# Kernel tuning notes

Hardware: AMD Instinct MI355X
Metric: run time of the kernel (lower is better)

The kernel has to match this reference:

```python
import jax, jax.numpy as jnp
from jax import lax
import numpy as np

B = 512          # batch
M = 2000         # num_memories
CC = 16          # conv_channel_size
F = CC * 4 * 6 * 6  # 2304 feature size
BN_EPS = 1e-5
COS_EPS = 1e-8
SHRINK_EPS = 0.01


def conv(x, w, b, stride, pad):
    y = lax.conv_general_dilated(x, w, (stride, stride), [(pad, pad), (pad, pad)],
                                 dimension_numbers=('NCHW', 'OIHW', 'NCHW'))
    return y + b[None, :, None, None]


def deconv(x, w, b, stride, pad, out_pad):
    # w is torch ConvTranspose2d layout: (in, out, kh, kw)
    k = w.shape[2]
    w2 = jnp.flip(w, (2, 3)).transpose(1, 0, 2, 3)  # (out, in, kh, kw)
    p = [(k - 1 - pad, k - 1 - pad + out_pad)] * 2
    y = lax.conv_general_dilated(x, w2, (1, 1), p, lhs_dilation=(stride, stride),
                                 dimension_numbers=('NCHW', 'OIHW', 'NCHW'))
    return y + b[None, :, None, None]


def bn(x, g, b):
    # BatchNorm2d in training mode: per-channel batch statistics (biased var)
    m = x.mean((0, 2, 3), keepdims=True)
    v = x.var((0, 2, 3), keepdims=True)
    return g[None, :, None, None] * (x - m) * lax.rsqrt(v + BN_EPS) + b[None, :, None, None]


def setup_inputs() -> dict:
    key = jax.random.key(0)
    ks = jax.random.split(key, 16)
    rn = lambda k, s, sc=0.05: jax.random.normal(k, s, jnp.float32) * sc
    return {
        'x': jax.random.uniform(ks[0], (B, 1, 96, 96), jnp.float32),
        'c1_w': rn(ks[1], (16, 1, 1, 1), 0.3), 'c1_b': jnp.zeros(16),
        'bn1_g': jnp.ones(16), 'bn1_b': jnp.zeros(16),
        'c2_w': rn(ks[2], (32, 16, 3, 3)), 'c2_b': jnp.zeros(32),
        'bn2_g': jnp.ones(32), 'bn2_b': jnp.zeros(32),
        'c3_w': rn(ks[3], (64, 32, 3, 3)), 'c3_b': jnp.zeros(64),
        'bn3_g': jnp.ones(64), 'bn3_b': jnp.zeros(64),
        'c4_w': rn(ks[4], (64, 64, 3, 3)), 'c4_b': jnp.zeros(64),
        'bn4_g': jnp.ones(64), 'bn4_b': jnp.zeros(64),
        'memory': rn(ks[5], (M, F), 0.03),
        'd0_w': rn(ks[6], (64, 64, 3, 3)), 'd0_b': jnp.zeros(64),
        'dbn0_g': jnp.ones(64), 'dbn0_b': jnp.zeros(64),
        'd1_w': rn(ks[7], (64, 32, 3, 3)), 'd1_b': jnp.zeros(32),
        'dbn1_g': jnp.ones(32), 'dbn1_b': jnp.zeros(32),
        'd2_w': rn(ks[8], (32, 16, 2, 2)), 'd2_b': jnp.zeros(16),
        'dbn2_g': jnp.ones(16), 'dbn2_b': jnp.zeros(16),
        'd3_w': rn(ks[9], (16, 1, 2, 2)), 'd3_b': jnp.zeros(1),
    }


def reference(x, c1_w, c1_b, bn1_g, bn1_b, c2_w, c2_b, bn2_g, bn2_b,
              c3_w, c3_b, bn3_g, bn3_b, c4_w, c4_b, bn4_g, bn4_b, memory,
              d0_w, d0_b, dbn0_g, dbn0_b, d1_w, d1_b, dbn1_g, dbn1_b,
              d2_w, d2_b, dbn2_g, dbn2_b, d3_w, d3_b):
    relu = jax.nn.relu
    # Encoder: 96 -> 49 -> 25 -> 13 -> 6
    h = relu(bn(conv(x, c1_w, c1_b, 2, 1), bn1_g, bn1_b))
    h = relu(bn(conv(h, c2_w, c2_b, 2, 1), bn2_g, bn2_b))
    h = relu(bn(conv(h, c3_w, c3_b, 2, 1), bn3_g, bn3_b))
    h = relu(bn(conv(h, c4_w, c4_b, 2, 0), bn4_g, bn4_b))
    z = h.reshape(h.shape[0], -1)  # (B, 2304)

    # Memory addressing: cosine similarity without materializing (B, M, F)
    zn = jnp.linalg.norm(z, axis=1)          # (B,)
    mn = jnp.linalg.norm(memory, axis=1)     # (M,)
    sim = (z @ memory.T) / jnp.maximum(zn[:, None] * mn[None, :], COS_EPS)
    w = jax.nn.softmax(sim, axis=1)
    # Sparse hard-shrink addressing + L1 renorm
    t = 1.0 / memory.shape[0]
    w = relu(w - t) * w / (jnp.abs(w - t) + SHRINK_EPS)
    w = w / jnp.sum(jnp.abs(w), axis=1, keepdims=True)
    z_hat = w @ memory  # (B, F)

    # Decoder: 6 -> 13 -> 25 -> 49 -> 98
    g = z_hat.reshape(-1, 64, 6, 6)
    g = relu(bn(deconv(g, d0_w, d0_b, 2, 0, 0), dbn0_g, dbn0_b))
    g = relu(bn(deconv(g, d1_w, d1_b, 2, 1, 0), dbn1_g, dbn1_b))
    g = relu(bn(deconv(g, d2_w, d2_b, 2, 1, 1), dbn2_g, dbn2_b))
    g = jax.nn.sigmoid(deconv(g, d3_w, d3_b, 2, 0, 0))
    return g
```

## Files before the change

kernel.cpp:

```cpp
#include <hip/hip_runtime.h>
#include <stdint.h>


typedef unsigned short ushort_t;
typedef __bf16 bf16x8 __attribute__((ext_vector_type(8)));
typedef float f32x4 __attribute__((ext_vector_type(4)));

#define DEV static __device__ __forceinline__

DEV ushort_t f2bf(float f){
  union { float f; uint32_t u; } v; v.f = f;
  return (ushort_t)((v.u + 0x7FFFu + ((v.u >> 16) & 1u)) >> 16);
}
DEV float bf2f(ushort_t u){
  union { uint32_t u; float f; } v; v.u = ((uint32_t)u) << 16;
  return v.f;
}

DEV uint32_t affine2(uint32_t rw, const float* ac, int ci, int nch){
  float lo = bf2f((ushort_t)(rw & 0xffffu));
  float hi = bf2f((ushort_t)(rw >> 16));
  lo = fmaxf(fmaf(ac[ci],   lo, ac[nch+ci]),   0.f);
  hi = fmaxf(fmaf(ac[ci+1], hi, ac[nch+ci+1]), 0.f);
  return (uint32_t)f2bf(lo) | ((uint32_t)f2bf(hi) << 16);
}
DEV uint4 stage_chunk(uint4 raw, const float* ac, int ci0, int nch){
  uint4 o;
  o.x = affine2(raw.x, ac, ci0+0, nch);
  o.y = affine2(raw.y, ac, ci0+2, nch);
  o.z = affine2(raw.z, ac, ci0+4, nch);
  o.w = affine2(raw.w, ac, ci0+6, nch);
  return o;
}

#define H_XS   0
#define H_S2   64
#define H_Q2   96
#define H_S3   192
#define H_Q3   256
#define H_S4   448
#define H_Q4   512
#define H_DS0  704
#define H_DQ0  768
#define H_DS1  960
#define H_DQ1  992
#define H_DS2  1088
#define H_DQ2  1104
#define H_ZN   1152
#define H_MN   1664
#define H_BUK  4096
#define NBUK   16
#define BSTRIDE 1280
#define HDR_FLOATS (H_BUK + NBUK*BSTRIDE)

#define OW2 0
#define OW3 5120
#define OW4 23552
#define OD0 60416
#define OD1 97280
#define OD2 115712
#define NWPK 117760

#define SIMSTRIDE 1024000
#define ZHSTRIDE  1179648
#define NSPL 4

#define PREP_XS 256
#define PREP_W2 (PREP_XS + 460)
#define PREP_TOT (PREP_W2 + 4536)

DEV float* bkt(float* hdr, int blk){ return hdr + H_BUK + (size_t)(blk & (NBUK-1))*BSTRIDE; }

DEV void coef_lds(const float* __restrict__ hdr, int offS, int offQ,
                  const float* __restrict__ g, const float* __restrict__ be,
                  float* ac, int nch, float invN, int tid){
  if (tid < nch){
    float s = 0.f, q = 0.f;
    #pragma unroll
    for (int k=0;k<NBUK;k++){
      s += hdr[H_BUK + k*BSTRIDE + offS + tid];
      q += hdr[H_BUK + k*BSTRIDE + offQ + tid];
    }
    float m = s*invN;
    float v = q*invN - m*m;
    float a = g[tid]*rsqrtf(v + 1e-5f);
    ac[tid] = a;
    ac[nch+tid] = be[tid] - m*a;
  }
}

__global__ __launch_bounds__(256) void k_prep(
    const float* __restrict__ mem, ushort_t* __restrict__ mbf, ushort_t* __restrict__ mt,
    float* __restrict__ hdr,
    const float* __restrict__ c2w, const float* __restrict__ c3w, const float* __restrict__ c4w,
    const float* __restrict__ d0w, const float* __restrict__ d1w, const float* __restrict__ d2w,
    ushort_t* __restrict__ WPK, const float* __restrict__ x){
  __shared__ float sm[32*33];
  const int blk = blockIdx.x, tid = threadIdx.x;
  if (blk < PREP_XS){
    float s = 0.f, q = 0.f;
    const int total = 512*49*49;
    for (int idx = blk*256 + tid; idx < total; idx += 256*256){
      int b = idx / 2401;
      int r = idx - b*2401;
      int i = r / 49, j = r - i*49;
      float v = 0.f;
      if (i > 0 && j > 0) v = x[(size_t)b*9216 + (2*i-1)*96 + (2*j-1)];
      s += v; q += v*v;
    }
    for (int o=32;o;o>>=1){ s += __shfl_down(s,o,64); q += __shfl_down(q,o,64); }
    int w = tid>>6;
    if ((tid&63)==0){ sm[w*2]=s; sm[w*2+1]=q; }
    __syncthreads();
    if (tid==0){
      float* bk = bkt(hdr, blk);
      atomicAdd(&bk[H_XS+0], sm[0]+sm[2]+sm[4]+sm[6]);
      atomicAdd(&bk[H_XS+1], sm[1]+sm[3]+sm[5]+sm[7]);
    }
  } else if (blk < PREP_W2){
    int i = (blk - PREP_XS)*256 + tid;
    if (i >= NWPK) return;
    float val = 0.f;
    if (i < OW3){
      int co = i/160, k = i - co*160, tap = k>>4, ci = k&15;
      if (tap < 9) val = c2w[(co*16+ci)*9+tap];
    } else if (i < OW4){
      int r = i - OW3; int co = r/288, k = r - co*288, tap = k>>5, ci = k&31;
      val = c3w[(co*32+ci)*9+tap];
    } else if (i < OD0){
      int r = i - OW4; int co = r/576, k = r - co*576, tap = k>>6, ci = k&63;
      val = c4w[(co*64+ci)*9+tap];
    } else if (i < OD1){
      int r = i - OD0;
      const int base[4]={0,16384,24576,32768}, K[4]={256,128,128,64};
      const int T0[4][4] = {{0,2,6,8},{1,7,0,0},{3,5,0,0},{4,0,0,0}};
      int cl = (r<16384)?0:(r<24576)?1:(r<32768)?2:3;
      int rr = r - base[cl]; int co = rr/K[cl], k = rr - co*K[cl], t = k>>6, ci = k&63;
      val = d0w[(ci*64+co)*9 + T0[cl][t]];
    } else if (i < OD2){
      int r = i - OD1;
      const int base[4]={0,2048,6144,10240}, K[4]={64,128,128,256};
      const int T1[4][4] = {{4,0,0,0},{3,5,0,0},{1,7,0,0},{0,2,6,8}};
      int cl = (r<2048)?0:(r<6144)?1:(r<10240)?2:3;
      int rr = r - base[cl]; int co = rr/K[cl], k = rr - co*K[cl], t = k>>6, ci = k&63;
      val = d1w[(ci*32+co)*9 + T1[cl][t]];
    } else {
      int r = i - OD2;
      int cl = r>>9, s = r&511, co = s>>5, ci = s&31;
      const int pis[4]={0,0,1,1}, pjs[4]={0,1,0,1};
      val = d2w[((ci*16+co)*2 + (1-pis[cl]))*2 + (1-pjs[cl])];
    }
    WPK[i] = f2bf(val);
  } else {
    const int mb = blk - PREP_W2;
    const int ft = mb % 72, mtile = mb / 72;
    const int tx = tid & 31, ty = tid >> 5;
    #pragma unroll
    for (int r0=0;r0<4;r0++){
      int m = mtile*32 + r0*8 + ty;
      int f = ft*32 + tx;
      float v = (m < 2000) ? mem[(size_t)m*2304 + f] : 0.f;
      sm[(r0*8+ty)*33 + tx] = v;
      if (m < 2000) mbf[(size_t)m*2304 + f] = f2bf(v);
      float p = v*v;
      for (int o=16;o;o>>=1) p += __shfl_down(p, o, 32);
      if (tx==0 && m<2000) atomicAdd(&hdr[H_MN+m], p);
    }
    __syncthreads();
    #pragma unroll
    for (int r0=0;r0<4;r0++){
      int f = ft*32 + r0*8 + ty;
      mt[(size_t)f*2016 + mtile*32 + tx] = f2bf(sm[tx*33 + r0*8+ty]);
    }
  }
}

__global__ __launch_bounds__(256) void k_conv2m(
    const float* __restrict__ x, const ushort_t* __restrict__ WPK, const float* __restrict__ b2g,
    const float* __restrict__ c1w, const float* __restrict__ c1b,
    const float* __restrict__ bn1g, const float* __restrict__ bn1b,
    float* __restrict__ hdr, ushort_t* __restrict__ out){
  __shared__ ushort_t inp[27*51*16];
  __shared__ float ac[32];
  const int blk = blockIdx.x, b = blk>>1, h = blk&1, tid = threadIdx.x;
  const int ro = h*13, nr = h?12:13, npos = nr*25, ntiles = (npos+15)>>4;
  if (tid < 16){
    float sx=0.f, qx=0.f;
    #pragma unroll
    for (int k=0;k<NBUK;k++){ sx += hdr[H_BUK+k*BSTRIDE+H_XS]; qx += hdr[H_BUK+k*BSTRIDE+H_XS+1]; }
    const float N = 512.f*49.f*49.f;
    float mx = sx/N, vx = qx/N - mx*mx;
    float mean = c1w[tid]*mx + c1b[tid];
    float a = bn1g[tid]*rsqrtf(c1w[tid]*c1w[tid]*vx + 1e-5f);
    ac[tid] = a*c1w[tid];
    ac[16+tid] = a*(c1b[tid]-mean) + bn1b[tid];
  }
  __syncthreads();
  for (int e = tid; e < 27*51; e += 256){
    int lr = e/51, gc = e - lr*51;
    int grg = 2*ro + lr;
    bool inside = (grg>=1 && grg<=49 && gc>=1 && gc<=49);
    float v = 0.f;
    if (grg>=2 && grg<=49 && gc>=2 && gc<=49) v = x[(size_t)b*9216 + (2*grg-3)*96 + (2*gc-3)];
    ushort_t hv[16];
    if (inside){
      #pragma unroll
      for (int c=0;c<16;c++) hv[c] = f2bf(fmaxf(fmaf(ac[c], v, ac[16+c]), 0.f));
    } else {
      #pragma unroll
      for (int c=0;c<16;c++) hv[c] = 0;
    }
    uint32_t w0[8];
    #pragma unroll
    for (int c=0;c<8;c++) w0[c] = (uint32_t)hv[2*c] | ((uint32_t)hv[2*c+1]<<16);
    uint4* dst = (uint4*)&inp[e*16];
    dst[0] = make_uint4(w0[0],w0[1],w0[2],w0[3]);
    dst[1] = make_uint4(w0[4],w0[5],w0[6],w0[7]);
  }
  __syncthreads();
  const int wv = tid>>6, lane = tid&63, r = lane&15, q = lane>>4;
  const int cotile = wv&1;
  bf16x8 af[5];
  #pragma unroll
  for (int c=0;c<5;c++) af[c] = *(const bf16x8*)(WPK + OW2 + (cotile*16+r)*160 + c*32 + q*8);
  float biasr[4];
  #pragma unroll
  for (int v=0;v<4;v++) biasr[v] = b2g[cotile*16 + q*4 + v];
  const int TOFF[10] = {0,1,2,51,52,53,102,103,104,0};
  const int qhi = q>>1, ci0 = (q&1)*8;
  float sacc[4]={0,0,0,0}, qacc[4]={0,0,0,0};
  for (int t = wv>>1; t < ntiles; t += 2){
    int p = t*16 + r;
    bool ok = p < npos;
    int pc = ok ? p : 0;
    int a_ = pc/25, c_ = pc - a_*25;
    int pb = (2*a_)*51 + 2*c_;
    f32x4 acc = {0.f,0.f,0.f,0.f};
    #pragma unroll
    for (int c=0;c<5;c++){
      int toff = qhi ? TOFF[2*c+1] : TOFF[2*c];
      bf16x8 bv = *(const bf16x8*)&inp[(pb + toff)*16 + ci0];
      acc = __builtin_amdgcn_mfma_f32_16x16x32_bf16(af[c], bv, acc, 0, 0, 0);
    }
    if (ok){
      int pg = (ro + a_)*25 + c_;
      ushort_t pk[4];
      #pragma unroll
      for (int reg=0;reg<4;reg++){
        float y = acc[reg] + biasr[reg];
        pk[reg] = f2bf(y);
        sacc[reg] += y; qacc[reg] += y*y;
      }
      *(uint2*)&out[((size_t)b*625 + pg)*32 + cotile*16 + q*4] =
        make_uint2((uint32_t)pk[0] | ((uint32_t)pk[1]<<16), (uint32_t)pk[2] | ((uint32_t)pk[3]<<16));
    }
  }
  float* bk = bkt(hdr, blk);
  #pragma unroll
  for (int reg=0;reg<4;reg++){
    float s = sacc[reg], qq = qacc[reg];
    for (int o=8;o;o>>=1){ s += __shfl_down(s,o,16); qq += __shfl_down(qq,o,16); }
    if (r==0){ atomicAdd(&bk[H_S2+cotile*16+q*4+reg], s); atomicAdd(&bk[H_Q2+cotile*16+q*4+reg], qq); }
  }
}

__global__ __launch_bounds__(256) void k_conv3m(
    const ushort_t* __restrict__ h2, const ushort_t* __restrict__ WPK, const float* __restrict__ b3g,
    const float* __restrict__ g, const float* __restrict__ be,
    float* __restrict__ hdr, ushort_t* __restrict__ out){
  __shared__ ushort_t inp[15*27*32];
  __shared__ float ac[64];
  const int blk = blockIdx.x, b = blk>>1, h = blk&1, tid = threadIdx.x;
  const int a0 = h*7, na = h?6:7, npos = na*13, ntiles = (npos+15)>>4, nrows = 2*na+1;
  coef_lds(hdr, H_S2, H_Q2, g, be, ac, 32, 1.f/(512.f*625.f), tid);
  __syncthreads();
  for (int e = tid; e < nrows*27*4; e += 256){
    int cell = e>>2, ch = e&3;
    int lr = cell/27, lc = cell - lr*27;
    int ii = 2*a0 - 1 + lr, j = lc - 1;
    uint4 val = make_uint4(0,0,0,0);
    if ((unsigned)ii < 25u && (unsigned)j < 25u){
      uint4 raw = *(const uint4*)&h2[((size_t)b*625 + ii*25 + j)*32 + ch*8];
      val = stage_chunk(raw, ac, ch*8, 32);
    }
    int slot = ch ^ ((cell>>1)&3);
    *(uint4*)&inp[cell*32 + slot*8] = val;
  }
  __syncthreads();
  const int wv = tid>>6, lane = tid&63, r = lane&15, q = lane>>4;
  bf16x8 af[9];
  #pragma unroll
  for (int c=0;c<9;c++) af[c] = *(const bf16x8*)(WPK + OW3 + (wv*16+r)*288 + c*32 + q*8);
  float biasr[4];
  #pragma unroll
  for (int v=0;v<4;v++) biasr[v] = b3g[wv*16 + q*4 + v];
  const int TOFF[9] = {0,1,2,27,28,29,54,55,56};
  float sacc[4]={0,0,0,0}, qacc[4]={0,0,0,0};
  for (int t = 0; t < ntiles; t++){
    int p = t*16 + r;
    bool ok = p < npos;
    int pc = ok ? p : 0;
    int a_ = pc/13, c_ = pc - a_*13;
    int pb = (2*a_)*27 + 2*c_;
    f32x4 acc = {0.f,0.f,0.f,0.f};
    #pragma unroll
    for (int c=0;c<9;c++){
      int cell = pb + TOFF[c];
      int slot = q ^ ((cell>>1)&3);
      bf16x8 bv = *(const bf16x8*)&inp[cell*32 + slot*8];
      acc = __builtin_amdgcn_mfma_f32_16x16x32_bf16(af[c], bv, acc, 0, 0, 0);
    }
    if (ok){
      int pos = (a0 + a_)*13 + c_;
      ushort_t pk[4];
      #pragma unroll
      for (int reg=0;reg<4;reg++){
        float y = acc[reg] + biasr[reg];
        pk[reg] = f2bf(y);
        sacc[reg] += y; qacc[reg] += y*y;
      }
      *(uint2*)&out[((size_t)b*169 + pos)*64 + wv*16 + q*4] =
        make_uint2((uint32_t)pk[0] | ((uint32_t)pk[1]<<16), (uint32_t)pk[2] | ((uint32_t)pk[3]<<16));
    }
  }
  float* bk = bkt(hdr, blk);
  #pragma unroll
  for (int reg=0;reg<4;reg++){
    float s = sacc[reg], qq = qacc[reg];
    for (int o=8;o;o>>=1){ s += __shfl_down(s,o,16); qq += __shfl_down(qq,o,16); }
    if (r==0){ atomicAdd(&bk[H_S3+wv*16+q*4+reg], s); atomicAdd(&bk[H_Q3+wv*16+q*4+reg], qq); }
  }
}

__global__ __launch_bounds__(256) void k_conv4m(
    const ushort_t* __restrict__ h3, const ushort_t* __restrict__ WPK, const float* __restrict__ b4g,
    const float* __restrict__ g, const float* __restrict__ be,
    float* __restrict__ hdr, float* __restrict__ out){
  __shared__ ushort_t inp[169*64];
  __shared__ float ac[128];
  const int b = blockIdx.x, tid = threadIdx.x;
  coef_lds(hdr, H_S3, H_Q3, g, be, ac, 64, 1.f/(512.f*169.f), tid);
  __syncthreads();
  for (int e = tid; e < 169*8; e += 256){
    int cell = e>>3, ch = e&7;
    uint4 raw = *(const uint4*)&h3[((size_t)b*169 + cell)*64 + ch*8];
    uint4 val = stage_chunk(raw, ac, ch*8, 64);
    int slot = ch ^ ((cell>>1)&7);
    *(uint4*)&inp[cell*64 + slot*8] = val;
  }
  __syncthreads();
  const int wv = tid>>6, lane = tid&63, r = lane&15, q = lane>>4;
  bf16x8 af[18];
  #pragma unroll
  for (int c=0;c<18;c++) af[c] = *(const bf16x8*)(WPK + OW4 + (wv*16+r)*576 + c*32 + q*8);
  float biasr[4];
  #pragma unroll
  for (int v=0;v<4;v++) biasr[v] = b4g[wv*16 + q*4 + v];
  const int TOFF[9] = {0,1,2,13,14,15,26,27,28};
  float sacc[4]={0,0,0,0}, qacc[4]={0,0,0,0};
  for (int t = 0; t < 3; t++){
    int p = t*16 + r;
    bool ok = p < 36;
    int pc = ok ? p : 0;
    int a_ = pc/6, c_ = pc - a_*6;
    int pb = (2*a_)*13 + 2*c_;
    f32x4 acc = {0.f,0.f,0.f,0.f};
    #pragma unroll
    for (int c=0;c<18;c++){
      int cell = pb + TOFF[c>>1];
      int chunk = (c&1)*4 + q;
      int slot = chunk ^ ((cell>>1)&7);
      bf16x8 bv = *(const bf16x8*)&inp[cell*64 + slot*8];
      acc = __builtin_amdgcn_mfma_f32_16x16x32_bf16(af[c], bv, acc, 0, 0, 0);
    }
    if (ok){
      #pragma unroll
      for (int reg=0;reg<4;reg++){
        float y = acc[reg] + biasr[reg];
        out[((size_t)b*64 + wv*16 + q*4 + reg)*36 + p] = y;
        sacc[reg] += y; qacc[reg] += y*y;
      }
    }
  }
  float* bk = bkt(hdr, b);
  #pragma unroll
  for (int reg=0;reg<4;reg++){
    float s = sacc[reg], qq = qacc[reg];
    for (int o=8;o;o>>=1){ s += __shfl_down(s,o,16); qq += __shfl_down(qq,o,16); }
    if (r==0){ atomicAdd(&bk[H_S4+wv*16+q*4+reg], s); atomicAdd(&bk[H_Q4+wv*16+q*4+reg], qq); }
  }
}

__global__ __launch_bounds__(256) void k_gemmA(
    const float* __restrict__ ZR, const ushort_t* __restrict__ Bm, float* __restrict__ D,
    const float* __restrict__ g, const float* __restrict__ be, float* __restrict__ hdr){
  __shared__ __align__(16) ushort_t lB[128*40];
  __shared__ __align__(16) ushort_t lA[128*40];
  __shared__ float ac[128];
  const int blk = blockIdx.x;
  const int s = blk >> 6, t = blk & 63;
  const int bi = t >> 4, bj = t & 15;
  const int m0 = bi*128, n0 = bj*128;
  const int k0 = s*18, k1 = k0 + 18;
  const int tid = threadIdx.x;
  coef_lds(hdr, H_S4, H_Q4, g, be, ac, 64, 1.f/(512.f*36.f), tid);
  const int lane = tid & 63, wv = tid >> 6;
  const int r = lane & 15, q = lane >> 4;
  const int wr = wv >> 1, wc = wv & 1;
  const bool bj0 = (bj == 0);
  float* Ds = D + (size_t)s*SIMSTRIDE;
  const int srow = tid >> 1, skq = (tid & 1) * 16;
  const bool bok = (n0 + srow) < 2000;
  const ushort_t* pb = Bm + (size_t)(n0 + srow)*2304 + skq;
  const float*    pa = ZR + (size_t)(m0 + srow)*2304 + skq;
  uint4* wB = (uint4*)&lB[srow*40 + skq];
  uint4* wA = (uint4*)&lA[srow*40 + skq];
  const uint4 zz = make_uint4(0,0,0,0);
  uint4 rb0 = bok ? *(const uint4*)(pb + (size_t)k0*32)     : zz;
  uint4 rb1 = bok ? *(const uint4*)(pb + (size_t)k0*32 + 8) : zz;
  f32x4 raA[4];
  #pragma unroll
  for (int i=0;i<4;i++) raA[i] = *(const f32x4*)(pa + (size_t)k0*32 + i*4);
  f32x4 acc[4][4];
  #pragma unroll
  for (int i=0;i<4;i++)
    #pragma unroll
    for (int j=0;j<4;j++) acc[i][j] = (f32x4){0.f,0.f,0.f,0.f};
  float zsq = 0.f;
  __syncthreads();
  for (int k=k0; k<k1; k++){
    if (k > k0) __syncthreads();
    wB[0] = rb0; wB[1] = rb1;
    {
      const int kb = k*32 + skq;
      uint32_t pw[8];
      #pragma unroll
      for (int jj=0;jj<8;jj++){
        float v0 = raA[jj>>1][(jj&1)*2+0];
        float v1 = raA[jj>>1][(jj&1)*2+1];
        int c0 = (kb + 2*jj) / 36;
        int c1 = (kb + 2*jj + 1) / 36;
        float h0 = fmaxf(fmaf(ac[c0], v0, ac[64+c0]), 0.f);
        float h1 = fmaxf(fmaf(ac[c1], v1, ac[64+c1]), 0.f);
        if (bj0) zsq += h0*h0 + h1*h1;
        pw[jj] = (uint32_t)f2bf(h0) | ((uint32_t)f2bf(h1) << 16);
      }
      wA[0] = make_uint4(pw[0],pw[1],pw[2],pw[3]);
      wA[1] = make_uint4(pw[4],pw[5],pw[6],pw[7]);
    }
    if (k+1 < k1){
      const ushort_t* nb = pb + (size_t)(k+1)*32;
      rb0 = bok ? *(const uint4*)(nb)     : zz;
      rb1 = bok ? *(const uint4*)(nb + 8) : zz;
      const float* na = pa + (size_t)(k+1)*32;
      #pragma unroll
      for (int i=0;i<4;i++) raA[i] = *(const f32x4*)(na + i*4);
    }
    __syncthreads();
    bf16x8 aF[4], bF[4];
    #pragma unroll
    for (int mt=0;mt<4;mt++) aF[mt] = *(const bf16x8*)&lA[(wr*64+mt*16+r)*40 + q*8];
    #pragma unroll
    for (int nt=0;nt<4;nt++) bF[nt] = *(const bf16x8*)&lB[(wc*64+nt*16+r)*40 + q*8];
    #pragma unroll
    for (int mt=0;mt<4;mt++)
      #pragma unroll
      for (int nt=0;nt<4;nt++)
        acc[mt][nt] = __builtin_amdgcn_mfma_f32_16x16x32_bf16(aF[mt], bF[nt], acc[mt][nt], 0, 0, 0);
  }
  if (bj0){
    zsq += __shfl_down(zsq, 1, 64);
    if ((tid & 1) == 0) atomicAdd(&hdr[H_ZN + m0 + srow], zsq);
  }
  #pragma unroll
  for (int mt=0;mt<4;mt++){
    int row = m0 + wr*64 + mt*16 + q*4;
    #pragma unroll
    for (int nt=0;nt<4;nt++){
      int col = n0 + wc*64 + nt*16 + r;
      if (col < 2000){
        #pragma unroll
        for (int reg=0;reg<4;reg++)
          Ds[(size_t)(row+reg)*2000 + col] = acc[mt][nt][reg];
      }
    }
  }
}

__global__ __launch_bounds__(256) void k_gemmB(const ushort_t* __restrict__ A, const ushort_t* __restrict__ Bm,
                                               float* __restrict__ D, int Nb, int N, int Kp, int kch,
                                               int tiles, int ksp, size_t dstride){
  __shared__ __align__(16) ushort_t lB[128*40];
  const int blk = blockIdx.x;
  const int s = blk / tiles, t = blk - s*tiles;
  const int bi = t / Nb, bj = t - bi*Nb;
  const int m0 = bi*128, n0 = bj*128;
  const int k0 = s*ksp, k1 = min(kch, k0 + ksp);
  const int tid = threadIdx.x;
  const int lane = tid & 63, wv = tid >> 6;
  const int r = lane & 15, q = lane >> 4;
  const int wr = wv >> 1, wc = wv & 1;
  float* Ds = D + (size_t)s*dstride;
  const int srow = tid >> 1, skq = (tid & 1) * 16;
  const bool bok = (n0 + srow) < N;
  const ushort_t* pb = Bm + (size_t)(n0 + srow)*Kp + skq;
  uint4* wB = (uint4*)&lB[srow*40 + skq];
  const uint4 zz = make_uint4(0,0,0,0);
  uint4 rb0 = bok ? *(const uint4*)(pb + k0*32)     : zz;
  uint4 rb1 = bok ? *(const uint4*)(pb + k0*32 + 8) : zz;
  const ushort_t* pa = A + (size_t)(m0 + wr*64 + r)*Kp + q*8;
  bf16x8 aN[4];
  #pragma unroll
  for (int mt=0;mt<4;mt++) aN[mt] = *(const bf16x8*)(pa + k0*32 + (size_t)(mt*16)*Kp);
  f32x4 acc[4][4];
  #pragma unroll
  for (int i=0;i<4;i++)
    #pragma unroll
    for (int j=0;j<4;j++) acc[i][j] = (f32x4){0.f,0.f,0.f,0.f};
  for (int k=k0; k<k1; k++){
    if (k > k0) __syncthreads();
    wB[0] = rb0; wB[1] = rb1;
    bf16x8 aF[4];
    #pragma unroll
    for (int mt=0;mt<4;mt++) aF[mt] = aN[mt];
    if (k+1 < k1){
      const ushort_t* nb = pb + (k+1)*32;
      rb0 = bok ? *(const uint4*)(nb)     : zz;
      rb1 = bok ? *(const uint4*)(nb + 8) : zz;
      const ushort_t* na = pa + (k+1)*32;
      #pragma unroll
      for (int mt=0;mt<4;mt++) aN[mt] = *(const bf16x8*)(na + (size_t)(mt*16)*Kp);
    }
    __syncthreads();
    bf16x8 bF[4];
    #pragma unroll
    for (int nt=0;nt<4;nt++) bF[nt] = *(const bf16x8*)&lB[(wc*64+nt*16+r)*40 + q*8];
    #pragma unroll
    for (int mt=0;mt<4;mt++)
      #pragma unroll
      for (int nt=0;nt<4;nt++)
        acc[mt][nt] = __builtin_amdgcn_mfma_f32_16x16x32_bf16(aF[mt], bF[nt], acc[mt][nt], 0, 0, 0);
  }
  #pragma unroll
  for (int mt=0;mt<4;mt++){
    int row = m0 + wr*64 + mt*16 + q*4;
    #pragma unroll
    for (int nt=0;nt<4;nt++){
      int col = n0 + wc*64 + nt*16 + r;
      if (col < N){
        #pragma unroll
        for (int reg=0;reg<4;reg++)
          Ds[(size_t)(row+reg)*N + col] = acc[mt][nt][reg];
      }
    }
  }
}

__global__ __launch_bounds__(256) void k_softmax(const float* __restrict__ sim, float* __restrict__ hdr,
                                                 ushort_t* __restrict__ wbf){
  __shared__ float e[2000];
  __shared__ float red[8];
  const int b = blockIdx.x, tid = threadIdx.x;
  const float znb = sqrtf(hdr[H_ZN+b]);
  float part = 0.f;
  for (int m=tid;m<2000;m+=256){
    size_t ix = (size_t)b*2000+m;
    float sv = 0.f;
    #pragma unroll
    for (int j=0;j<NSPL;j++) sv += sim[ix + (size_t)j*SIMSTRIDE];
    float mnb = sqrtf(hdr[H_MN+m]);
    float s = sv / fmaxf(znb * mnb, 1e-8f);
    float ev = __expf(s);
    e[m] = ev; part += ev;
  }
  for (int o=32;o;o>>=1) part += __shfl_down(part,o,64);
  if ((tid&63)==0) red[tid>>6] = part;
  __syncthreads();
  const float denom = red[0]+red[1]+red[2]+red[3];
  const float t = 1.0f/2000.0f;
  float part2 = 0.f;
  for (int m=tid;m<2000;m+=256){
    float w = e[m]/denom;
    float d = w - t;
    float sh = fmaxf(d,0.f)*w/(fabsf(d)+0.01f);
    e[m] = sh; part2 += sh;
  }
  for (int o=32;o;o>>=1) part2 += __shfl_down(part2,o,64);
  if ((tid&63)==0) red[4+(tid>>6)] = part2;
  __syncthreads();
  const float inv = 1.0f/(red[4]+red[5]+red[6]+red[7]);
  for (int m=tid;m<2016;m+=256){
    ushort_t o = 0;
    if (m < 2000) o = f2bf(e[m]*inv);
    wbf[(size_t)b*2016+m] = o;
  }
}

__global__ __launch_bounds__(256) void k_deconv0m(
    const float* __restrict__ zh, const ushort_t* __restrict__ WPK, const float* __restrict__ b0g,
    float* __restrict__ hdr, ushort_t* __restrict__ out){
  __shared__ ushort_t inp[64*64];
  const int b = blockIdx.x, tid = threadIdx.x;
  for (int i = tid; i < 512; i += 256) ((uint4*)inp)[i] = make_uint4(0,0,0,0);
  __syncthreads();
  for (int i = tid; i < 576; i += 256){
    int idx = i*4;
    f32x4 v = *(const f32x4*)&zh[(size_t)b*2304 + idx];
    #pragma unroll
    for (int j=1;j<NSPL;j++)
      v += *(const f32x4*)&zh[(size_t)b*2304 + idx + (size_t)j*ZHSTRIDE];
    int ci = idx/36;
    int p  = idx - ci*36;
    int chunk = ci >> 3, cil = ci & 7;
    #pragma unroll
    for (int e2=0;e2<4;e2++){
      int pp = p + e2;
      int r6 = pp/6, c6 = pp - r6*6;
      int cell = (r6+1)*8 + (c6+1);
      int slot = chunk ^ ((cell>>1)&7);
      inp[cell*64 + slot*8 + cil] = f2bf(v[e2]);
    }
  }
  __syncthreads();
  const int wv = tid>>6, lane = tid&63, r = lane&15, q = lane>>4;
  float biasr[4];
  #pragma unroll
  for (int v=0;v<4;v++) biasr[v] = b0g[wv*16 + q*4 + v];
  const int NCOL[4]={7,6,7,6}, NPOS[4]={49,42,42,36}, NT[4]={4,3,3,3},
            NCH[4]={8,4,4,2}, KB[4]={0,16384,24576,32768}, KK[4]={256,128,128,64},
            PI[4]={0,0,1,1}, PJ[4]={0,1,0,1};
  const int TOFF[4][4] = {{9,8,1,0},{9,1,0,0},{9,8,0,0},{9,0,0,0}};
  float sacc[4]={0,0,0,0}, qacc[4]={0,0,0,0};
  #pragma unroll
  for (int cl=0; cl<4; cl++){
    bf16x8 af[8];
    #pragma unroll
    for (int m=0;m<NCH[cl];m++)
      af[m] = *(const bf16x8*)(WPK + OD0 + KB[cl] + (wv*16+r)*KK[cl] + m*32 + q*8);
    for (int t = 0; t < NT[cl]; t++){
      int p = t*16 + r;
      bool ok = p < NPOS[cl];
      int pc = ok ? p : 0;
      int a_ = pc/NCOL[cl], c_ = pc - a_*NCOL[cl];
      int pb = a_*8 + c_;
      f32x4 acc = {0.f,0.f,0.f,0.f};
      #pragma unroll
      for (int m=0;m<NCH[cl];m++){
        int cell = pb + TOFF[cl][m>>1];
        int chunk = (m&1)*4 + q;
        int slot = chunk ^ ((cell>>1)&7);
        bf16x8 bv = *(const bf16x8*)&inp[cell*64 + slot*8];
        acc = __builtin_amdgcn_mfma_f32_16x16x32_bf16(af[m], bv, acc, 0, 0, 0);
      }
      if (ok){
        int pos = (2*a_+PI[cl])*13 + (2*c_+PJ[cl]);
        ushort_t pk[4];
        #pragma unroll
        for (int reg=0;reg<4;reg++){
          float y = acc[reg] + biasr[reg];
          pk[reg] = f2bf(y);
          sacc[reg] += y; qacc[reg] += y*y;
        }
        *(uint2*)&out[((size_t)b*169 + pos)*64 + wv*16 + q*4] =
          make_uint2((uint32_t)pk[0] | ((uint32_t)pk[1]<<16), (uint32_t)pk[2] | ((uint32_t)pk[3]<<16));
      }
    }
  }
  float* bk = bkt(hdr, b);
  #pragma unroll
  for (int reg=0;reg<4;reg++){
    float s = sacc[reg], qq = qacc[reg];
    for (int o=8;o;o>>=1){ s += __shfl_down(s,o,16); qq += __shfl_down(qq,o,16); }
    if (r==0){ atomicAdd(&bk[H_DS0+wv*16+q*4+reg], s); atomicAdd(&bk[H_DQ0+wv*16+q*4+reg], qq); }
  }
}

__global__ __launch_bounds__(256) void k_deconv1m(
    const ushort_t* __restrict__ g0, const ushort_t* __restrict__ WPK, const float* __restrict__ b1g,
    const float* __restrict__ g, const float* __restrict__ be,
    float* __restrict__ hdr, ushort_t* __restrict__ out){
  __shared__ ushort_t inp[169*64];
  __shared__ float ac[128];
  const int b = blockIdx.x, tid = threadIdx.x;
  coef_lds(hdr, H_DS0, H_DQ0, g, be, ac, 64, 1.f/(512.f*169.f), tid);
  __syncthreads();
  for (int e = tid; e < 169*8; e += 256){
    int cell = e>>3, ch = e&7;
    uint4 raw = *(const uint4*)&g0[((size_t)b*169 + cell)*64 + ch*8];
    uint4 val = stage_chunk(raw, ac, ch*8, 64);
    int slot = ch ^ ((cell>>1)&7);
    *(uint4*)&inp[cell*64 + slot*8] = val;
  }
  __syncthreads();
  const int wv = tid>>6, lane = tid&63, r = lane&15, q = lane>>4;
  const int cotile = wv&1, ph = wv>>1;
  float biasr[4];
  #pragma unroll
  for (int v=0;v<4;v++) biasr[v] = b1g[cotile*16 + q*4 + v];
  const int NCOL[4]={13,12,13,12}, NPOS[4]={169,156,156,144}, NT[4]={11,10,10,9},
            NCH[4]={2,4,4,8}, KB[4]={0,2048,6144,10240}, KK[4]={64,128,128,256},
            PI[4]={0,0,1,1}, PJ[4]={0,1,0,1};
  const int TOFF[4][4] = {{0,0,0,0},{1,0,0,0},{13,0,0,0},{14,13,1,0}};
  float sacc[4]={0,0,0,0}, qacc[4]={0,0,0,0};
  #pragma unroll
  for (int cl=0; cl<4; cl++){
    bf16x8 af[8];
    #pragma unroll
    for (int m=0;m<NCH[cl];m++)
      af[m] = *(const bf16x8*)(WPK + OD1 + KB[cl] + (cotile*16+r)*KK[cl] + m*32 + q*8);
    for (int t = ph; t < NT[cl]; t += 2){
      int p = t*16 + r;
      bool ok = p < NPOS[cl];
      int pc = ok ? p : 0;
      int a_ = pc/NCOL[cl], c_ = pc - a_*NCOL[cl];
      int pb = a_*13 + c_;
      f32x4 acc = {0.f,0.f,0.f,0.f};
      #pragma unroll
      for (int m=0;m<NCH[cl];m++){
        int cell = pb + TOFF[cl][m>>1];
        int chunk = (m&1)*4 + q;
        int slot = chunk ^ ((cell>>1)&7);
        bf16x8 bv = *(const bf16x8*)&inp[cell*64 + slot*8];
        acc = __builtin_amdgcn_mfma_f32_16x16x32_bf16(af[m], bv, acc, 0, 0, 0);
      }
      if (ok){
        int pos = (2*a_+PI[cl])*25 + (2*c_+PJ[cl]);
        ushort_t pk[4];
        #pragma unroll
        for (int reg=0;reg<4;reg++){
          float y = acc[reg] + biasr[reg];
          pk[reg] = f2bf(y);
          sacc[reg] += y; qacc[reg] += y*y;
        }
        *(uint2*)&out[((size_t)b*625 + pos)*32 + cotile*16 + q*4] =
          make_uint2((uint32_t)pk[0] | ((uint32_t)pk[1]<<16), (uint32_t)pk[2] | ((uint32_t)pk[3]<<16));
      }
    }
  }
  float* bk = bkt(hdr, b);
  #pragma unroll
  for (int reg=0;reg<4;reg++){
    float s = sacc[reg], qq = qacc[reg];
    for (int o=8;o;o>>=1){ s += __shfl_down(s,o,16); qq += __shfl_down(qq,o,16); }
    if (r==0){ atomicAdd(&bk[H_DS1+cotile*16+q*4+reg], s); atomicAdd(&bk[H_DQ1+cotile*16+q*4+reg], qq); }
  }
}

__global__ __launch_bounds__(256) void k_deconv2m(
    const ushort_t* __restrict__ g1, const ushort_t* __restrict__ WPK, const float* __restrict__ bg,
    const float* __restrict__ g, const float* __restrict__ be,
    float* __restrict__ hdr, ushort_t* __restrict__ out){
  __shared__ ushort_t inp[625*32];
  __shared__ float ac[64];
  const int b = blockIdx.x, tid = threadIdx.x;
  coef_lds(hdr, H_DS1, H_DQ1, g, be, ac, 32, 1.f/(512.f*625.f), tid);
  __syncthreads();
  for (int e = tid; e < 625*4; e += 256){
    int cell = e>>2, ch = e&3;
    uint4 raw = *(const uint4*)&g1[((size_t)b*625 + cell)*32 + ch*8];
    uint4 val = stage_chunk(raw, ac, ch*8, 32);
    int slot = ch ^ ((cell>>1)&3);
    *(uint4*)&inp[cell*32 + slot*8] = val;
  }
  __syncthreads();
  const int wv = tid>>6, lane = tid&63, r = lane&15, q = lane>>4;
  const int cl = wv;
  float biasr[4];
  #pragma unroll
  for (int v=0;v<4;v++) biasr[v] = bg[q*4 + v];
  const int NCOL[4]={25,24,25,24}, NPOS[4]={625,600,600,576}, NT[4]={40,38,38,36},
            TOFF[4]={0,1,25,26};
  const int nc = NCOL[cl], npos = NPOS[cl], nt = NT[cl], toff = TOFF[cl];
  bf16x8 af = *(const bf16x8*)(WPK + OD2 + cl*512 + r*32 + q*8);
  float sacc[4]={0,0,0,0}, qacc[4]={0,0,0,0};
  for (int t = 0; t < nt; t++){
    int p = t*16 + r;
    bool ok = p < npos;
    int pc = ok ? p : 0;
    int a_ = pc/nc, c_ = pc - a_*nc;
    int cell = a_*25 + c_ + toff;
    int slot = q ^ ((cell>>1)&3);
    f32x4 acc = {0.f,0.f,0.f,0.f};
    bf16x8 bv = *(const bf16x8*)&inp[cell*32 + slot*8];
    acc = __builtin_amdgcn_mfma_f32_16x16x32_bf16(af, bv, acc, 0, 0, 0);
    if (ok){
      #pragma unroll
      for (int reg=0;reg<4;reg++){
        float y = acc[reg] + biasr[reg];
        out[((size_t)(b*16 + q*4 + reg)*4 + cl)*625 + p] = f2bf(y);
        sacc[reg] += y; qacc[reg] += y*y;
      }
    }
  }
  float* bk = bkt(hdr, b);
  #pragma unroll
  for (int reg=0;reg<4;reg++){
    float s = sacc[reg], qq = qacc[reg];
    for (int o=8;o;o>>=1){ s += __shfl_down(s,o,16); qq += __shfl_down(qq,o,16); }
    if (r==0){ atomicAdd(&bk[H_DS2+q*4+reg], s); atomicAdd(&bk[H_DQ2+q*4+reg], qq); }
  }
}

__global__ __launch_bounds__(256) void k_deconv3(const ushort_t* __restrict__ g2, const float* __restrict__ w,
                                                 const float* __restrict__ bias,
                                                 const float* __restrict__ g, const float* __restrict__ be,
                                                 float* __restrict__ hdr, float* __restrict__ out){
  __shared__ float ac[32];
  __shared__ float wl[64];
  const int tid = threadIdx.x;
  coef_lds(hdr, H_DS2, H_DQ2, g, be, ac, 16, 1.f/(512.f*2401.f), tid);
  if (tid >= 64 && tid < 128) wl[tid-64] = w[tid-64];
  __syncthreads();
  int idx = blockIdx.x*256 + tid;
  if (idx >= 512*2401) return;
  int b = idx / 2401; int loc = idx - b*2401;
  int ii = loc / 49, jj = loc - ii*49;
  int pi = ii & 1, pj = jj & 1, cl = pi*2 + pj;
  int a = ii >> 1, c = jj >> 1;
  int nc = pj ? 24 : 25;
  const float b0 = bias[0];
  float acc00 = b0, acc01 = b0, acc10 = b0, acc11 = b0;
  const ushort_t* gp = g2 + ((size_t)(b*16)*4 + cl)*625 + a*nc + c;
  #pragma unroll
  for (int ci=0; ci<16; ci++){
    float raw = bf2f(gp[(size_t)ci*4*625]);
    float h = fmaxf(fmaf(ac[ci], raw, ac[16+ci]), 0.f);
    acc00 = fmaf(h, wl[ci*4+0], acc00);
    acc01 = fmaf(h, wl[ci*4+1], acc01);
    acc10 = fmaf(h, wl[ci*4+2], acc10);
    acc11 = fmaf(h, wl[ci*4+3], acc11);
  }
  float* op = out + (size_t)b*9604 + (2*ii)*98 + 2*jj;
  op[0]   = 1.f/(1.f + __expf(-acc00));
  op[1]   = 1.f/(1.f + __expf(-acc01));
  op[98]  = 1.f/(1.f + __expf(-acc10));
  op[99]  = 1.f/(1.f + __expf(-acc11));
}

extern "C" void kernel_launch(void* const* d_in, const int* in_sizes, int n_in,
                              void* d_out, int out_size, void* d_ws, size_t ws_size,
                              hipStream_t stream){
  (void)in_sizes; (void)n_in; (void)out_size; (void)ws_size;
  const float* x     = (const float*)d_in[0];
  const float* c1w   = (const float*)d_in[1];
  const float* c1b   = (const float*)d_in[2];
  const float* bn1g  = (const float*)d_in[3];
  const float* bn1b  = (const float*)d_in[4];
  const float* c2w   = (const float*)d_in[5];
  const float* c2b   = (const float*)d_in[6];
  const float* bn2g  = (const float*)d_in[7];
  const float* bn2b  = (const float*)d_in[8];
  const float* c3w   = (const float*)d_in[9];
  const float* c3b   = (const float*)d_in[10];
  const float* bn3g  = (const float*)d_in[11];
  const float* bn3b  = (const float*)d_in[12];
  const float* c4w   = (const float*)d_in[13];
  const float* c4b   = (const float*)d_in[14];
  const float* bn4g  = (const float*)d_in[15];
  const float* bn4b  = (const float*)d_in[16];
  const float* mem   = (const float*)d_in[17];
  const float* d0w   = (const float*)d_in[18];
  const float* d0b   = (const float*)d_in[19];
  const float* dbn0g = (const float*)d_in[20];
  const float* dbn0b = (const float*)d_in[21];
  const float* d1w   = (const float*)d_in[22];
  const float* d1b   = (const float*)d_in[23];
  const float* dbn1g = (const float*)d_in[24];
  const float* dbn1b = (const float*)d_in[25];
  const float* d2w   = (const float*)d_in[26];
  const float* d2b   = (const float*)d_in[27];
  const float* dbn2g = (const float*)d_in[28];
  const float* dbn2b = (const float*)d_in[29];
  const float* d3w   = (const float*)d_in[30];
  const float* d3b   = (const float*)d_in[31];

  float* hdr  = (float*)d_ws;
  float* H2f  = hdr + HDR_FLOATS;
  float* H3f  = H2f + 10240000;
  float* ZRAW = H3f + 5537792;
  float* WSLOT= ZRAW + 1179648;
  float* G2   = WSLOT + 73728;
  ushort_t* MEMBF = (ushort_t*)(G2 + 19668992);
  ushort_t* MEMT  = MEMBF + 4608000;
  ushort_t* ZBF   = MEMT + 4644864;
  ushort_t* WBF   = ZBF + 1179648;
  ushort_t* WPK   = (ushort_t*)WSLOT;
  float* SIMP = G2;
  float* ZHP  = G2 + NSPL*SIMSTRIDE;
  ushort_t* G2BF = (ushort_t*)G2;
  ushort_t* H2CL = (ushort_t*)H2f;
  ushort_t* H3CL = (ushort_t*)H3f;
  ushort_t* G0CL = (ushort_t*)H3f;
  ushort_t* G1CL = (ushort_t*)H2f;
  float* OUT = (float*)d_out;

  hipMemsetAsync(hdr, 0, HDR_FLOATS*sizeof(float), stream);
  k_prep     <<<PREP_TOT, 256, 0, stream>>>(mem, MEMBF, MEMT, hdr,
                                            c2w, c3w, c4w, d0w, d1w, d2w, WPK, x);
  k_conv2m   <<<1024, 256, 0, stream>>>(x, WPK, c2b, c1w, c1b, bn1g, bn1b, hdr, H2CL);
  k_conv3m   <<<1024, 256, 0, stream>>>(H2CL, WPK, c3b, bn2g, bn2b, hdr, H3CL);
  k_conv4m   <<<512, 256, 0, stream>>>(H3CL, WPK, c4b, bn3g, bn3b, hdr, ZRAW);
  k_gemmA    <<<256, 256, 0, stream>>>(ZRAW, MEMBF, SIMP, bn4g, bn4b, hdr);
  k_softmax  <<<512, 256, 0, stream>>>(SIMP, hdr, WBF);
  k_gemmB    <<<288, 256, 0, stream>>>(WBF, MEMT, ZHP, 18, 2304, 2016, 63, 72, 16, ZHSTRIDE);
  k_deconv0m <<<512, 256, 0, stream>>>(ZHP, WPK, d0b, hdr, G0CL);
  k_deconv1m <<<512, 256, 0, stream>>>(G0CL, WPK, d1b, dbn0g, dbn0b, hdr, G1CL);
  k_deconv2m <<<512, 256, 0, stream>>>(G1CL, WPK, d2b, dbn1g, dbn1b, hdr, G2BF);
  k_deconv3  <<<4802, 256, 0, stream>>>(G2BF, d3w, d3b, dbn2g, dbn2b, hdr, OUT);
}
```

Measured before the change: 346.2 us.

## Vectorize memory prep transpose and switch deconv2 output to channel-last layout

The memory prep kernel now reads four floats per thread, packs them to bf16 before staging in shared memory, and handles 128-feature tiles per block, so fewer blocks are launched and global accesses are wider. The deconv2 output is changed from channel-planar to position-major with 16 channels contiguous. This lets deconv2 write 8-byte packed stores and lets the final deconv read all 16 channels with two 16-byte loads instead of 16 strided scalar loads. The transpose step still does 2-byte scalar global stores, and the shared-memory reads in that loop may hit bank conflicts.

```diff
diff --git a/kernel.cpp b/kernel.cpp
--- a/kernel.cpp
+++ b/kernel.cpp
@@ -67,7 +67,7 @@
 
 #define PREP_XS 256
 #define PREP_W2 (PREP_XS + 460)
-#define PREP_TOT (PREP_W2 + 4536)
+#define PREP_TOT (PREP_W2 + 63*18)
 
 DEV float* bkt(float* hdr, int blk){ return hdr + H_BUK + (size_t)(blk & (NBUK-1))*BSTRIDE; }
 
@@ -95,9 +95,10 @@
     const float* __restrict__ c2w, const float* __restrict__ c3w, const float* __restrict__ c4w,
     const float* __restrict__ d0w, const float* __restrict__ d1w, const float* __restrict__ d2w,
     ushort_t* __restrict__ WPK, const float* __restrict__ x){
-  __shared__ float sm[32*33];
+  __shared__ ushort_t smu[32*132];
   const int blk = blockIdx.x, tid = threadIdx.x;
   if (blk < PREP_XS){
+    float* sm = (float*)smu;
     float s = 0.f, q = 0.f;
     const int total = 512*49*49;
     for (int idx = blk*256 + tid; idx < total; idx += 256*256){
@@ -153,24 +154,27 @@
     WPK[i] = f2bf(val);
   } else {
     const int mb = blk - PREP_W2;
-    const int ft = mb % 72, mtile = mb / 72;
+    const int ft = mb % 18, mtile = mb / 18;
     const int tx = tid & 31, ty = tid >> 5;
     #pragma unroll
     for (int r0=0;r0<4;r0++){
       int m = mtile*32 + r0*8 + ty;
-      int f = ft*32 + tx;
-      float v = (m < 2000) ? mem[(size_t)m*2304 + f] : 0.f;
-      sm[(r0*8+ty)*33 + tx] = v;
-      if (m < 2000) mbf[(size_t)m*2304 + f] = f2bf(v);
-      float p = v*v;
+      int f = ft*128 + tx*4;
+      f32x4 v = {0.f,0.f,0.f,0.f};
+      if (m < 2000) v = *(const f32x4*)&mem[(size_t)m*2304 + f];
+      ushort_t h0=f2bf(v[0]), h1=f2bf(v[1]), h2=f2bf(v[2]), h3=f2bf(v[3]);
+      uint2 pk = make_uint2((uint32_t)h0 | ((uint32_t)h1<<16), (uint32_t)h2 | ((uint32_t)h3<<16));
+      *(uint2*)&smu[(r0*8+ty)*132 + tx*4] = pk;
+      if (m < 2000) *(uint2*)&mbf[(size_t)m*2304 + f] = pk;
+      float p = v[0]*v[0] + v[1]*v[1] + v[2]*v[2] + v[3]*v[3];
       for (int o=16;o;o>>=1) p += __shfl_down(p, o, 32);
       if (tx==0 && m<2000) atomicAdd(&hdr[H_MN+m], p);
     }
     __syncthreads();
     #pragma unroll
-    for (int r0=0;r0<4;r0++){
-      int f = ft*32 + r0*8 + ty;
-      mt[(size_t)f*2016 + mtile*32 + tx] = f2bf(sm[tx*33 + r0*8+ty]);
+    for (int ff=0; ff<16; ff++){
+      int fl = ff*8 + ty;
+      mt[(size_t)(ft*128 + fl)*2016 + mtile*32 + tx] = smu[tx*132 + fl];
     }
   }
 }
@@ -784,12 +788,15 @@
     bf16x8 bv = *(const bf16x8*)&inp[cell*32 + slot*8];
     acc = __builtin_amdgcn_mfma_f32_16x16x32_bf16(af, bv, acc, 0, 0, 0);
     if (ok){
+      ushort_t pk[4];
       #pragma unroll
       for (int reg=0;reg<4;reg++){
         float y = acc[reg] + biasr[reg];
-        out[((size_t)(b*16 + q*4 + reg)*4 + cl)*625 + p] = f2bf(y);
+        pk[reg] = f2bf(y);
         sacc[reg] += y; qacc[reg] += y*y;
       }
+      *(uint2*)&out[(((size_t)b*4 + cl)*625 + p)*16 + q*4] =
+        make_uint2((uint32_t)pk[0] | ((uint32_t)pk[1]<<16), (uint32_t)pk[2] | ((uint32_t)pk[3]<<16));
     }
   }
   float* bk = bkt(hdr, b);
@@ -820,10 +827,13 @@
   int nc = pj ? 24 : 25;
   const float b0 = bias[0];
   float acc00 = b0, acc01 = b0, acc10 = b0, acc11 = b0;
-  const ushort_t* gp = g2 + ((size_t)(b*16)*4 + cl)*625 + a*nc + c;
+  const ushort_t* gp = g2 + (((size_t)b*4 + cl)*625 + a*nc + c)*16;
+  ushort_t rv[16];
+  *(uint4*)&rv[0] = *(const uint4*)(gp);
+  *(uint4*)&rv[8] = *(const uint4*)(gp + 8);
   #pragma unroll
   for (int ci=0; ci<16; ci++){
-    float raw = bf2f(gp[(size_t)ci*4*625]);
+    float raw = bf2f(rv[ci]);
     float h = fmaxf(fmaf(ac[ci], raw, ac[16+ci]), 0.f);
     acc00 = fmaf(h, wl[ci*4+0], acc00);
     acc01 = fmaf(h, wl[ci*4+1], acc01);
```

After: 321.5 us. -7.1%, faster.
